# Kernel optimization log

Hardware: AMD Instinct MI355X
Metric: run time of the kernel (lower is better)

Reference implementation:

```python
import jax, jax.numpy as jnp
import numpy as np

B, N, NP, K, C_IN, C, H = 16, 4096, 1024, 32, 128, 256, 4
C_G = C_IN + 3  # grouped feature dim (use_xyz concat of relative coords)
EPS = 1e-3      # keras LayerNormalization default epsilon


def setup_inputs() -> dict:
    key = jax.random.key(0)
    ks = jax.random.split(key, 16)
    s = 0.05
    return {
        "xyz": jax.random.normal(ks[0], (B, N, 3), jnp.float32),
        "newxyz": jax.random.normal(ks[1], (B, NP, 3), jnp.float32),
        "feature_input": jax.random.normal(ks[2], (B, N, C_IN), jnp.float32),
        "w_qkv": jax.random.normal(ks[3], (C_G, 3 * C), jnp.float32) * s,
        "proj_w": jax.random.normal(ks[4], (C, C), jnp.float32) * s,
        "proj_b": jnp.zeros((C,), jnp.float32),
        "dense_w": jax.random.normal(ks[5], (C_G, C), jnp.float32) * s,
        "dense_b": jnp.zeros((C,), jnp.float32),
        "fc1_w": jax.random.normal(ks[6], (C, 2 * C), jnp.float32) * s,
        "fc1_b": jnp.zeros((2 * C,), jnp.float32),
        "fc2_w": jax.random.normal(ks[7], (2 * C, C), jnp.float32) * s,
        "fc2_b": jnp.zeros((C,), jnp.float32),
        "n1_g": jnp.ones((C_G,), jnp.float32),
        "n1_b": jnp.zeros((C_G,), jnp.float32),
        "n2_g": jnp.ones((C,), jnp.float32),
        "n2_b": jnp.zeros((C,), jnp.float32),
        "group_num": K,
        "training": True,
    }


def _layernorm(x, g, b):
    m = jnp.mean(x, axis=-1, keepdims=True)
    v = jnp.mean(jnp.square(x - m), axis=-1, keepdims=True)
    return (x - m) * jax.lax.rsqrt(v + EPS) * g + b


def _sample_and_group(newxyz, group_num, xyz, feats):
    # squared pairwise distances (B, NP, N)
    d2 = (jnp.sum(newxyz**2, -1)[:, :, None]
          - 2.0 * jnp.einsum('bpc,bnc->bpn', newxyz, xyz)
          + jnp.sum(xyz**2, -1)[:, None, :])
    _, idx = jax.lax.top_k(-d2, group_num)            # (B, NP, K) nearest
    b_idx = jnp.arange(newxyz.shape[0])[:, None, None]
    grouped_xyz = xyz[b_idx, idx] - newxyz[:, :, None, :]   # (B, NP, K, 3)
    grouped_feat = feats[b_idx, idx]                        # (B, NP, K, C_IN)
    return jnp.concatenate([grouped_xyz, grouped_feat], axis=-1)


def _self_attention(x, w_qkv, proj_w, proj_b):
    b, n, k = x.shape[0], x.shape[1], x.shape[2]
    d = C // H
    qkv = jnp.einsum('bnkc,cd->bnkd', x, w_qkv)
    qkv = qkv.reshape(b, n, k, 3, H, d)
    qkv = jnp.transpose(qkv, (3, 0, 1, 4, 2, 5))      # (3, B, NP, H, K, d)
    q, kk, v = qkv[0], qkv[1], qkv[2]
    qm = jnp.max(q, axis=-2, keepdims=True)           # (B, NP, H, 1, d)
    attn = jnp.einsum('bnhqd,bnhkd->bnhqk', qm, kk) * (C ** -0.5)
    attn = jax.nn.softmax(attn, axis=-1)
    out = jnp.einsum('bnhqk,bnhkd->bnhqd', attn, v)[..., 0, :]  # (B, NP, H, d)
    out = out.reshape(b, n, C)
    return jax.nn.relu(out @ proj_w + proj_b)


def reference(xyz, newxyz, feature_input, w_qkv, proj_w, proj_b, dense_w,
              dense_b, fc1_w, fc1_b, fc2_w, fc2_b, n1_g, n1_b, n2_g, n2_b,
              group_num, training):
    gf = _sample_and_group(newxyz, group_num, xyz, feature_input)  # (B,NP,K,C_G)
    feat = _self_attention(_layernorm(gf, n1_g, n1_b), w_qkv, proj_w, proj_b)
    feat = feat + jax.nn.relu(jnp.max(gf, axis=-2) @ dense_w + dense_b)
    f2 = _layernorm(feat, n2_g, n2_b)
    f2 = jax.nn.relu(f2 @ fc1_w + fc1_b)
    f2 = f2 @ fc2_w + fc2_b
    return f2 + feat
```

## Files before the change

### kernel.cpp

```cpp
#include <hip/hip_runtime.h>
#include <hip/hip_bf16.h>

typedef __hip_bfloat16 bf16;

#define Bn   16
#define Nn   4096
#define NPn  1024
#define Kn   32
#define CINn 128
#define CGn  131
#define Cn   256
#define Hn   4
#define KPAD 160
#define XBS  168
#define XFS2 136
#define GFS  136

typedef __attribute__((ext_vector_type(8))) short frag_ab;
typedef __attribute__((ext_vector_type(4))) float frag_cd;

__device__ __forceinline__ float b2f(bf16 x) { return __bfloat162float(x); }
__device__ __forceinline__ bf16  f2b(float x) { return __float2bfloat16(x); }
__device__ __forceinline__ short f2bs(float x) {
  union { bf16 h; short s; } u; u.h = __float2bfloat16(x); return u.s;
}
__device__ __forceinline__ float bs2f(short s) {
  union { short v; bf16 h; } u; u.v = s; return __bfloat162float(u.h);
}
__device__ __forceinline__ unsigned f2ord(float f) {
  unsigned u = __float_as_uint(f);
  return u ^ ((u >> 31) ? 0xffffffffu : 0x80000000u);
}

__global__ __launch_bounds__(256) void xyzw_prep_kernel(
    const float* __restrict__ xyz, float4* __restrict__ xyzw) {
  const int i = blockIdx.x * 256 + threadIdx.x;
  const float x = xyz[i*3 + 0];
  const float y = xyz[i*3 + 1];
  const float z = xyz[i*3 + 2];
  const float sx = __fadd_rn(__fadd_rn(__fmul_rn(x,x), __fmul_rn(y,y)),
                             __fmul_rn(z,z));
  xyzw[i] = make_float4(x, y, z, sx);
}

__global__ __launch_bounds__(256) void knn_kernel(const float4* __restrict__ xyzw,
                                                  const float* __restrict__ newxyz,
                                                  int* __restrict__ idx_out) {
  constexpr int CAP = 2048;
  __shared__ unsigned long long tmin[256];
  __shared__ __align__(16) unsigned long long cand[CAP + 4];
  __shared__ unsigned long long wtau[4];
  __shared__ unsigned long long wred[4];
  __shared__ int scnt;
  const int bp  = blockIdx.x;
  const int b   = bp >> 10;
  const int tid = threadIdx.x;
  const float qx = newxyz[bp*3 + 0];
  const float qy = newxyz[bp*3 + 1];
  const float qz = newxyz[bp*3 + 2];
  const float sn = __fadd_rn(__fadd_rn(__fmul_rn(qx,qx), __fmul_rn(qy,qy)),
                             __fmul_rn(qz,qz));
  const float4* xb = xyzw + (size_t)b * Nn;
  unsigned long long key[16];
  unsigned long long lmin = ~0ull;
  #pragma unroll
  for (int s = 0; s < 16; ++s) {
    const int n = s*256 + tid;
    const float4 xw = xb[n];
    const float dot = __fadd_rn(__fadd_rn(__fmul_rn(qx,xw.x), __fmul_rn(qy,xw.y)),
                                __fmul_rn(qz,xw.z));
    const float d2 = __fadd_rn(__fsub_rn(sn, __fmul_rn(2.0f, dot)), xw.w);
    key[s] = ((unsigned long long)f2ord(d2) << 32) | (unsigned)n;
    if (key[s] < lmin) lmin = key[s];
  }
  const int lane = tid & 63, wv = tid >> 6;

  if (tid == 0) scnt = 0;
  tmin[tid] = lmin;
  __syncthreads();

  {
    const unsigned long long* wt = &tmin[wv * 64];
    int rk = 0;
    #pragma unroll 8
    for (int j = 0; j < 64; ++j) rk += (wt[j] < lmin) ? 1 : 0;
    if (rk == 15) wtau[wv] = lmin;
  }
  __syncthreads();
  unsigned long long tau = wtau[0];
  if (wtau[1] < tau) tau = wtau[1];
  if (wtau[2] < tau) tau = wtau[2];
  if (wtau[3] < tau) tau = wtau[3];

  #pragma unroll
  for (int s = 0; s < 16; ++s) {
    if (key[s] <= tau) {
      const int p = atomicAdd(&scnt, 1);
      if (p < CAP) cand[p] = key[s];
    }
  }
  __syncthreads();
  const int m = scnt;

  if (m >= Kn && m <= CAP) {
    if (tid < 4) cand[m + tid] = ~0ull;
    __syncthreads();
    const int m4 = (m + 3) & ~3;
    for (int t = tid; t < m; t += 256) {
      const unsigned long long mykey = cand[t];
      int r = 0;
      for (int j = 0; j < m4; j += 4) {
        r += (cand[j+0] < mykey) ? 1 : 0;
        r += (cand[j+1] < mykey) ? 1 : 0;
        r += (cand[j+2] < mykey) ? 1 : 0;
        r += (cand[j+3] < mykey) ? 1 : 0;
      }
      if (r < Kn) idx_out[(size_t)bp*Kn + r] = (int)(mykey & 0xffffffffu);
    }
  } else {
    for (int s = 0; s < Kn; ++s) {
      unsigned long long mm = lmin;
      #pragma unroll
      for (int d = 32; d; d >>= 1) {
        const unsigned lo = __shfl_xor((unsigned)(mm & 0xffffffffu), d, 64);
        const unsigned hi = __shfl_xor((unsigned)(mm >> 32), d, 64);
        const unsigned long long o = ((unsigned long long)hi << 32) | lo;
        if (o < mm) mm = o;
      }
      if (lane == 0) wred[wv] = mm;
      __syncthreads();
      unsigned long long best = wred[0];
      if (wred[1] < best) best = wred[1];
      if (wred[2] < best) best = wred[2];
      if (wred[3] < best) best = wred[3];
      __syncthreads();
      const int n = (int)(best & 0xffffffffu);
      if (tid == 0) idx_out[(size_t)bp*Kn + s] = n;
      if ((n & 255) == tid) {
        const int slot = n >> 8;
        #pragma unroll
        for (int t = 0; t < 16; ++t) if (t == slot) key[t] = ~0ull;
        unsigned long long m2 = ~0ull;
        #pragma unroll
        for (int t = 0; t < 16; ++t) if (key[t] < m2) m2 = key[t];
        lmin = m2;
      }
    }
  }
}

__global__ __launch_bounds__(256) void wprep_all_kernel(
    const float* __restrict__ w_qkv, const float* __restrict__ proj_w,
    const float* __restrict__ dense_w, const float* __restrict__ fc1_w,
    const float* __restrict__ fc2_w, short* __restrict__ o_qkv,
    short* __restrict__ o_proj, short* __restrict__ o_dense,
    short* __restrict__ o_fc1, short* __restrict__ o_fc2) {
  const int blk = blockIdx.x;
  const float* W; short* out; int K, N, nnt, remap, base;
  if      (blk <  480) { W=w_qkv;   out=o_qkv;   K=CGn; N=768; nnt=48; remap=1; base=0;    }
  else if (blk <  736) { W=proj_w;  out=o_proj;  K=Cn;  N=256; nnt=16; remap=0; base=480;  }
  else if (blk <  896) { W=dense_w; out=o_dense; K=CGn; N=256; nnt=16; remap=1; base=736;  }
  else if (blk < 1408) { W=fc1_w;   out=o_fc1;   K=Cn;  N=512; nnt=32; remap=0; base=896;  }
  else                 { W=fc2_w;   out=o_fc2;   K=512; N=256; nnt=16; remap=0; base=1408; }
  const int t = (blk - base) * 256 + threadIdx.x;
  const int j    = t & 7;
  const int lane = (t >> 3) & 63;
  const int nt   = (t >> 9) % nnt;
  const int kt   = (t >> 9) / nnt;
  const int k = kt*32 + (lane >> 4)*8 + j;
  const int n = nt*16 + (lane & 15);
  int krow = k;
  if (remap) krow = (k < 128) ? k + 3 : k - 128;
  out[t] = (k < K) ? f2bs(W[(size_t)krow*N + n]) : (short)0;
}

__global__ __launch_bounds__(256, 3) void fused_attn_kernel(
    const float* __restrict__ xyz, const float* __restrict__ newxyz,
    const float* __restrict__ featin, const short* __restrict__ wfrag,
    const float* __restrict__ n1g, const float* __restrict__ n1b,
    const int* __restrict__ idx, bf16* __restrict__ attnout,
    bf16* __restrict__ gfmax) {
  __shared__ __align__(16) short Raw[64 * XFS2];
  __shared__ __align__(16) short Xs[64 * XBS];
  __shared__ float sg[CGn], sb[CGn];
  __shared__ int sidx[64];
  const int bp0 = blockIdx.x * 2;
  const int b   = bp0 >> 10;
  const int tid = threadIdx.x;
  if (tid < 64) {
    int n = idx[(size_t)bp0*Kn + tid];
    sidx[tid] = ((unsigned)n < (unsigned)Nn) ? n : 0;
  }
  if (tid < CGn) {
    const int rj = (tid < 128) ? tid + 3 : tid - 128;
    sg[tid] = n1g[rj];
    sb[tid] = n1b[rj];
  }
  __syncthreads();
  const int kk = tid >> 3, sub = tid & 7;
  const int lane = tid & 63, w = tid >> 6;
  const int col = lane & 15, quad = lane >> 4;
  float mean[2], rstd[2];
  {
    float4 r[2][4];
    float ex[2] = {0.f, 0.f};
    #pragma unroll
    for (int p = 0; p < 2; ++p) {
      const int row = p*32 + kk;
      const float* frow = featin + ((size_t)b*Nn + sidx[row])*CINn;
      #pragma unroll
      for (int i = 0; i < 4; ++i) r[p][i] = *(const float4*)(frow + sub*4 + 32*i);
      if (sub < 3)
        ex[p] = xyz[((size_t)b*Nn + sidx[row])*3 + sub] - newxyz[(bp0+p)*3 + sub];
    }
    #pragma unroll
    for (int p = 0; p < 2; ++p) {
      const int row = p*32 + kk;
      #pragma unroll
      for (int i = 0; i < 4; ++i) {
        short4 s4 = { f2bs(r[p][i].x), f2bs(r[p][i].y), f2bs(r[p][i].z), f2bs(r[p][i].w) };
        *(short4*)&Raw[row*XFS2 + sub*4 + 32*i] = s4;
      }
      if (sub < 3) Raw[row*XFS2 + 128 + sub] = f2bs(ex[p]);
    }
    #pragma unroll
    for (int p = 0; p < 2; ++p) {
      float s = ex[p], s2 = ex[p]*ex[p];
      #pragma unroll
      for (int i = 0; i < 4; ++i) {
        s  += r[p][i].x + r[p][i].y + r[p][i].z + r[p][i].w;
        s2 += r[p][i].x*r[p][i].x + r[p][i].y*r[p][i].y
            + r[p][i].z*r[p][i].z + r[p][i].w*r[p][i].w;
      }
      s  += __shfl_xor(s, 1, 64);  s  += __shfl_xor(s, 2, 64);  s  += __shfl_xor(s, 4, 64);
      s2 += __shfl_xor(s2, 1, 64); s2 += __shfl_xor(s2, 2, 64); s2 += __shfl_xor(s2, 4, 64);
      mean[p] = s * (1.0f/CGn);
      const float var = s2 * (1.0f/CGn) - mean[p]*mean[p];
      rstd[p] = rsqrtf(var + 1e-3f);
    }
  }
  __syncthreads();
  #pragma unroll
  for (int p = 0; p < 2; ++p) {
    if (tid < GFS) {
      float m = 0.f;
      if (tid < CGn) {
        m = -1e30f;
        #pragma unroll
        for (int k2 = 0; k2 < Kn; ++k2)
          m = fmaxf(m, bs2f(Raw[(p*32 + k2)*XFS2 + tid]));
      }
      gfmax[(size_t)(bp0+p)*GFS + tid] = f2b(m);
    }
  }
  #pragma unroll
  for (int p = 0; p < 2; ++p) {
    const int row = p*32 + kk;
    #pragma unroll
    for (int i = 0; i < 4; ++i) {
      const float4 g4 = *(const float4*)&sg[sub*4 + 32*i];
      const float4 b4 = *(const float4*)&sb[sub*4 + 32*i];
      const short4 rv = *(const short4*)&Raw[row*XFS2 + sub*4 + 32*i];
      short4 s4;
      s4.x = f2bs((bs2f(rv.x) - mean[p])*rstd[p]*g4.x + b4.x);
      s4.y = f2bs((bs2f(rv.y) - mean[p])*rstd[p]*g4.y + b4.y);
      s4.z = f2bs((bs2f(rv.z) - mean[p])*rstd[p]*g4.z + b4.z);
      s4.w = f2bs((bs2f(rv.w) - mean[p])*rstd[p]*g4.w + b4.w);
      *(short4*)&Xs[row*XBS + sub*4 + 32*i] = s4;
    }
    if (sub < 3) {
      const float rxv = bs2f(Raw[row*XFS2 + 128 + sub]);
      Xs[row*XBS + 128 + sub] = f2bs((rxv - mean[p])*rstd[p]*sg[128+sub] + sb[128+sub]);
    }
  }
  #pragma unroll
  for (int u = 0; u < 8; ++u) {
    const int e = u*256 + tid;
    const int row = e >> 5, jj = 131 + (e & 31);
    if (jj < 160) Xs[row*XBS + jj] = 0;
  }
  __syncthreads();
  float qm[2][4], aw[2][2][4], inv[2];
  {
    #pragma unroll 1
    for (int half = 0; half < 2; ++half) {
      frag_cd acc[2][4] = {};
      for (int kt = 0; kt < 5; ++kt) {
        const int ko = kt*32 + quad*8;
        frag_ab a[4];
        #pragma unroll
        for (int mt = 0; mt < 4; ++mt)
          a[mt] = *(const frag_ab*)&Xs[(mt*16 + col)*XBS + ko];
        #pragma unroll
        for (int ntl = 0; ntl < 2; ++ntl) {
          const int nt = w*4 + half*2 + ntl;
          const frag_ab bfr = *(const frag_ab*)(wfrag + ((size_t)(kt*48 + nt)*64 + lane)*8);
          #pragma unroll
          for (int mt = 0; mt < 4; ++mt)
            acc[ntl][mt] = __builtin_amdgcn_mfma_f32_16x16x32_bf16(a[mt], bfr, acc[ntl][mt], 0, 0, 0);
        }
      }
      #pragma unroll
      for (int p = 0; p < 2; ++p)
        #pragma unroll
        for (int ntl = 0; ntl < 2; ++ntl) {
          float m = -1e30f;
          #pragma unroll
          for (int mtl = 0; mtl < 2; ++mtl)
            #pragma unroll
            for (int rr = 0; rr < 4; ++rr) m = fmaxf(m, acc[ntl][p*2+mtl][rr]);
          m = fmaxf(m, __shfl_xor(m, 16, 64));
          m = fmaxf(m, __shfl_xor(m, 32, 64));
          qm[p][half*2 + ntl] = m;
        }
    }
  }
  {
    float pp[2][2][4] = {};
    #pragma unroll 1
    for (int half = 0; half < 2; ++half) {
      frag_cd acc[2][4] = {};
      for (int kt = 0; kt < 5; ++kt) {
        const int ko = kt*32 + quad*8;
        frag_ab a[4];
        #pragma unroll
        for (int mt = 0; mt < 4; ++mt)
          a[mt] = *(const frag_ab*)&Xs[(mt*16 + col)*XBS + ko];
        #pragma unroll
        for (int ntl = 0; ntl < 2; ++ntl) {
          const int nt = 16 + w*4 + half*2 + ntl;
          const frag_ab bfr = *(const frag_ab*)(wfrag + ((size_t)(kt*48 + nt)*64 + lane)*8);
          #pragma unroll
          for (int mt = 0; mt < 4; ++mt)
            acc[ntl][mt] = __builtin_amdgcn_mfma_f32_16x16x32_bf16(a[mt], bfr, acc[ntl][mt], 0, 0, 0);
        }
      }
      #pragma unroll
      for (int p = 0; p < 2; ++p)
        #pragma unroll
        for (int mtl = 0; mtl < 2; ++mtl)
          #pragma unroll
          for (int rr = 0; rr < 4; ++rr) {
            #pragma unroll
            for (int ntl = 0; ntl < 2; ++ntl)
              pp[p][mtl][rr] = fmaf(qm[p][half*2 + ntl], acc[ntl][p*2+mtl][rr], pp[p][mtl][rr]);
          }
    }
    #pragma unroll
    for (int p = 0; p < 2; ++p) {
      float lg[2][4];
      #pragma unroll
      for (int mtl = 0; mtl < 2; ++mtl)
        #pragma unroll
        for (int rr = 0; rr < 4; ++rr) {
          float v = pp[p][mtl][rr];
          #pragma unroll
          for (int d = 1; d < 16; d <<= 1) v += __shfl_xor(v, d, 64);
          lg[mtl][rr] = v * 0.0625f;
        }
      float mx = -1e30f;
      #pragma unroll
      for (int mtl = 0; mtl < 2; ++mtl)
        #pragma unroll
        for (int rr = 0; rr < 4; ++rr) mx = fmaxf(mx, lg[mtl][rr]);
      mx = fmaxf(mx, __shfl_xor(mx, 16, 64));
      mx = fmaxf(mx, __shfl_xor(mx, 32, 64));
      float ssum = 0.f;
      #pragma unroll
      for (int mtl = 0; mtl < 2; ++mtl)
        #pragma unroll
        for (int rr = 0; rr < 4; ++rr) { aw[p][mtl][rr] = expf(lg[mtl][rr] - mx); ssum += aw[p][mtl][rr]; }
      ssum += __shfl_xor(ssum, 16, 64);
      ssum += __shfl_xor(ssum, 32, 64);
      inv[p] = 1.f / ssum;
    }
  }
  {
    #pragma unroll 1
    for (int half = 0; half < 2; ++half) {
      frag_cd acc[2][4] = {};
      for (int kt = 0; kt < 5; ++kt) {
        const int ko = kt*32 + quad*8;
        frag_ab a[4];
        #pragma unroll
        for (int mt = 0; mt < 4; ++mt)
          a[mt] = *(const frag_ab*)&Xs[(mt*16 + col)*XBS + ko];
        #pragma unroll
        for (int ntl = 0; ntl < 2; ++ntl) {
          const int nt = 32 + w*4 + half*2 + ntl;
          const frag_ab bfr = *(const frag_ab*)(wfrag + ((size_t)(kt*48 + nt)*64 + lane)*8);
          #pragma unroll
          for (int mt = 0; mt < 4; ++mt)
            acc[ntl][mt] = __builtin_amdgcn_mfma_f32_16x16x32_bf16(a[mt], bfr, acc[ntl][mt], 0, 0, 0);
        }
      }
      #pragma unroll
      for (int p = 0; p < 2; ++p)
        #pragma unroll
        for (int ntl = 0; ntl < 2; ++ntl) {
          float o = 0.f;
          #pragma unroll
          for (int mtl = 0; mtl < 2; ++mtl)
            #pragma unroll
            for (int rr = 0; rr < 4; ++rr) o = fmaf(aw[p][mtl][rr], acc[ntl][p*2+mtl][rr], o);
          o += __shfl_xor(o, 16, 64);
          o += __shfl_xor(o, 32, 64);
          if (quad == 0)
            attnout[(size_t)(bp0+p)*Cn + w*64 + (half*2 + ntl)*16 + col] = f2b(o * inv[p]);
        }
    }
  }
}

template<bool RELU, bool ADD_S, bool OUT_BF16>
__global__ __launch_bounds__(256) void mfma_gemm_kernel(
    const bf16* __restrict__ A, int lda, int Ka,
    const short* __restrict__ Wf, int nnt_total, int N,
    const float* __restrict__ bias, const bf16* __restrict__ S,
    void* __restrict__ Dv) {
  __shared__ __align__(16) short As[64*40];
  const int m0 = blockIdx.y * 64;
  const int n0 = blockIdx.x * 128;
  const int tid = threadIdx.x, lane = tid & 63, w = tid >> 6;
  const int col = lane & 15, quad = lane >> 4;
  const int row = tid >> 2, c8 = (tid & 3) * 8;
  frag_cd acc[4][2] = {};
  const int nkt = (Ka + 31) >> 5;
  for (int kt = 0; kt < nkt; ++kt) {
    const int k0 = kt*32 + c8;
    frag_ab av = {0,0,0,0,0,0,0,0};
    if (k0 + 8 <= Ka)
      av = *(const frag_ab*)((const short*)A + (size_t)(m0+row)*lda + k0);
    __syncthreads();
    *(frag_ab*)&As[row*40 + c8] = av;
    __syncthreads();
    frag_ab afr[4];
    #pragma unroll
    for (int mt = 0; mt < 4; ++mt)
      afr[mt] = *(const frag_ab*)&As[(mt*16 + col)*40 + quad*8];
    #pragma unroll
    for (int ntl = 0; ntl < 2; ++ntl) {
      const int nt = (n0 >> 4) + w*2 + ntl;
      const frag_ab bfr = *(const frag_ab*)(Wf + ((size_t)(kt*nnt_total + nt)*64 + lane)*8);
      #pragma unroll
      for (int mt = 0; mt < 4; ++mt)
        acc[mt][ntl] = __builtin_amdgcn_mfma_f32_16x16x32_bf16(afr[mt], bfr, acc[mt][ntl], 0, 0, 0);
    }
  }
  #pragma unroll
  for (int ntl = 0; ntl < 2; ++ntl) {
    const int n = n0 + w*32 + ntl*16 + col;
    const float bv = bias[n];
    #pragma unroll
    for (int mt = 0; mt < 4; ++mt) {
      #pragma unroll
      for (int r = 0; r < 4; ++r) {
        const int m = m0 + mt*16 + quad*4 + r;
        float v = acc[mt][ntl][r] + bv;
        if (RELU) v = fmaxf(v, 0.f);
        if (ADD_S) v += b2f(S[(size_t)m*N + n]);
        if (OUT_BF16) ((bf16*)Dv)[(size_t)m*N + n] = f2b(v);
        else          ((float*)Dv)[(size_t)m*N + n] = v;
      }
    }
  }
}

__global__ __launch_bounds__(256) void dual_gemm_kernel(
    const bf16* __restrict__ A1, const short* __restrict__ W1,
    const bf16* __restrict__ A2, const short* __restrict__ W2,
    const float* __restrict__ b1, const float* __restrict__ b2,
    bf16* __restrict__ D) {
  __shared__ __align__(16) short As[64*40];
  const int m0 = blockIdx.y * 64;
  const int n0 = blockIdx.x * 128;
  const int tid = threadIdx.x, lane = tid & 63, w = tid >> 6;
  const int col = lane & 15, quad = lane >> 4;
  const int row = tid >> 2, c8 = (tid & 3) * 8;
  frag_cd acc1[4][2] = {}, acc2[4][2] = {};
  for (int kt = 0; kt < 8; ++kt) {
    const frag_ab av = *(const frag_ab*)((const short*)A1 + (size_t)(m0+row)*Cn + kt*32 + c8);
    __syncthreads();
    *(frag_ab*)&As[row*40 + c8] = av;
    __syncthreads();
    frag_ab afr[4];
    #pragma unroll
    for (int mt = 0; mt < 4; ++mt)
      afr[mt] = *(const frag_ab*)&As[(mt*16 + col)*40 + quad*8];
    #pragma unroll
    for (int ntl = 0; ntl < 2; ++ntl) {
      const int nt = (n0 >> 4) + w*2 + ntl;
      const frag_ab bfr = *(const frag_ab*)(W1 + ((size_t)(kt*16 + nt)*64 + lane)*8);
      #pragma unroll
      for (int mt = 0; mt < 4; ++mt)
        acc1[mt][ntl] = __builtin_amdgcn_mfma_f32_16x16x32_bf16(afr[mt], bfr, acc1[mt][ntl], 0, 0, 0);
    }
  }
  for (int kt = 0; kt < 5; ++kt) {
    const int k0 = kt*32 + c8;
    frag_ab av = {0,0,0,0,0,0,0,0};
    if (k0 + 8 <= GFS)
      av = *(const frag_ab*)((const short*)A2 + (size_t)(m0+row)*GFS + k0);
    __syncthreads();
    *(frag_ab*)&As[row*40 + c8] = av;
    __syncthreads();
    frag_ab afr[4];
    #pragma unroll
    for (int mt = 0; mt < 4; ++mt)
      afr[mt] = *(const frag_ab*)&As[(mt*16 + col)*40 + quad*8];
    #pragma unroll
    for (int ntl = 0; ntl < 2; ++ntl) {
      const int nt = (n0 >> 4) + w*2 + ntl;
      const frag_ab bfr = *(const frag_ab*)(W2 + ((size_t)(kt*16 + nt)*64 + lane)*8);
      #pragma unroll
      for (int mt = 0; mt < 4; ++mt)
        acc2[mt][ntl] = __builtin_amdgcn_mfma_f32_16x16x32_bf16(afr[mt], bfr, acc2[mt][ntl], 0, 0, 0);
    }
  }
  #pragma unroll
  for (int ntl = 0; ntl < 2; ++ntl) {
    const int n = n0 + w*32 + ntl*16 + col;
    const float bv1 = b1[n], bv2 = b2[n];
    #pragma unroll
    for (int mt = 0; mt < 4; ++mt) {
      #pragma unroll
      for (int r = 0; r < 4; ++r) {
        const int m = m0 + mt*16 + quad*4 + r;
        const float v = fmaxf(acc1[mt][ntl][r] + bv1, 0.f)
                      + fmaxf(acc2[mt][ntl][r] + bv2, 0.f);
        D[(size_t)m*Cn + n] = f2b(v);
      }
    }
  }
}

__global__ __launch_bounds__(256) void ln2_kernel(const bf16* __restrict__ feat,
                                                  const float* __restrict__ g,
                                                  const float* __restrict__ b,
                                                  bf16* __restrict__ out) {
  const int r = blockIdx.x*4 + (threadIdx.x >> 6), lane = threadIdx.x & 63;
  float vv[4];
  #pragma unroll
  for (int c = 0; c < 4; ++c) vv[c] = b2f(feat[(size_t)r*Cn + lane*4 + c]);
  float s  = vv[0] + vv[1] + vv[2] + vv[3];
  float s2 = vv[0]*vv[0] + vv[1]*vv[1] + vv[2]*vv[2] + vv[3]*vv[3];
  #pragma unroll
  for (int d = 32; d; d >>= 1) { s += __shfl_xor(s, d, 64); s2 += __shfl_xor(s2, d, 64); }
  const float mean = s * (1.f/256.f);
  const float var  = s2 * (1.f/256.f) - mean*mean;
  const float rstd = rsqrtf(var + 1e-3f);
  #pragma unroll
  for (int c = 0; c < 4; ++c) {
    const int cc = lane*4 + c;
    out[(size_t)r*Cn + cc] = f2b((vv[c] - mean)*rstd*g[cc] + b[cc]);
  }
}

extern "C" void kernel_launch(void* const* d_in, const int* in_sizes, int n_in,
                              void* d_out, int out_size, void* d_ws, size_t ws_size,
                              hipStream_t stream) {
  const float* xyz     = (const float*)d_in[0];
  const float* newxyz  = (const float*)d_in[1];
  const float* featin  = (const float*)d_in[2];
  const float* w_qkv   = (const float*)d_in[3];
  const float* proj_w  = (const float*)d_in[4];
  const float* proj_b  = (const float*)d_in[5];
  const float* dense_w = (const float*)d_in[6];
  const float* dense_b = (const float*)d_in[7];
  const float* fc1_w   = (const float*)d_in[8];
  const float* fc1_b   = (const float*)d_in[9];
  const float* fc2_w   = (const float*)d_in[10];
  const float* fc2_b   = (const float*)d_in[11];
  const float* n1g     = (const float*)d_in[12];
  const float* n1b     = (const float*)d_in[13];
  const float* n2g     = (const float*)d_in[14];
  const float* n2b     = (const float*)d_in[15];

  char*  ws     = (char*)d_ws;
  short* wqkv   = (short*)(ws + 0);
  short* wproj  = (short*)(ws + 245760);
  short* wdense = (short*)(ws + 376832);
  short* wfc1   = (short*)(ws + 458752);
  short* wfc2   = (short*)(ws + 720896);
  bf16*  featB  = (bf16*)(ws + 1048576);
  bf16*  attnA  = (bf16*)(ws + 9437184);
  bf16*  gfmax  = (bf16*)(ws + 17825792);
  int*   idxws  = (int*) (ws + 22282240);
  bf16*  fc1out = (bf16*)(ws + 24379392);
  float4* xyzw  = (float4*)(ws + 24379392);

  const int M = Bn * NPn;

  xyzw_prep_kernel<<<dim3(Bn*Nn/256), dim3(256), 0, stream>>>(xyz, xyzw);
  knn_kernel<<<dim3(M), dim3(256), 0, stream>>>(xyzw, newxyz, idxws);
  wprep_all_kernel<<<dim3(1920), dim3(256), 0, stream>>>(
      w_qkv, proj_w, dense_w, fc1_w, fc2_w, wqkv, wproj, wdense, wfc1, wfc2);

  fused_attn_kernel<<<dim3(M/2), dim3(256), 0, stream>>>(
      xyz, newxyz, featin, wqkv, n1g, n1b, idxws, attnA, gfmax);
  dual_gemm_kernel<<<dim3(2, M/64), dim3(256), 0, stream>>>(
      attnA, wproj, gfmax, wdense, proj_b, dense_b, featB);
  ln2_kernel<<<dim3(M/4), dim3(256), 0, stream>>>(featB, n2g, n2b, attnA);
  mfma_gemm_kernel<true, false, true><<<dim3(4, M/64), dim3(256), 0, stream>>>(
      attnA, Cn, Cn, wfc1, 32, 512, fc1_b, (const bf16*)nullptr, fc1out);
  mfma_gemm_kernel<false, true, false><<<dim3(2, M/64), dim3(256), 0, stream>>>(
      fc1out, 512, 512, wfc2, 16, Cn, fc2_b, featB, d_out);
}
```

Baseline: 421.2 us.

## Batch eight queries per KNN block and drop separate raw LDS buffer

The KNN kernel now handles eight query points per block and keeps the batch's 4096 reference points in registers across those queries, so the point data is loaded once per block rather than once per query. In the fused attention kernel, the separate Raw LDS buffer is removed: raw bf16 features are staged in Xs for the group-max, and the layernorm is then computed from the fp32 values held in registers, with an extra barrier before Xs is overwritten. This lowers LDS usage and may raise occupancy, and the layernorm input is now fp32 instead of bf16-rounded. The costs are more register pressure (16 float4 per thread in KNN), fewer KNN blocks to spread across the GPU, and queries inside a block running one after another.

```diff
diff --git a/kernel.cpp b/kernel.cpp
--- a/kernel.cpp
+++ b/kernel.cpp
@@ -15,6 +15,7 @@
 #define XBS  168
 #define XFS2 136
 #define GFS  136
+#define KNNG 8
 
 typedef __attribute__((ext_vector_type(8))) short frag_ab;
 typedef __attribute__((ext_vector_type(4))) float frag_cd;
@@ -52,99 +53,108 @@
   __shared__ unsigned long long wtau[4];
   __shared__ unsigned long long wred[4];
   __shared__ int scnt;
-  const int bp  = blockIdx.x;
-  const int b   = bp >> 10;
+  const int bp0 = blockIdx.x * KNNG;
+  const int b   = bp0 >> 10;
   const int tid = threadIdx.x;
-  const float qx = newxyz[bp*3 + 0];
-  const float qy = newxyz[bp*3 + 1];
-  const float qz = newxyz[bp*3 + 2];
-  const float sn = __fadd_rn(__fadd_rn(__fmul_rn(qx,qx), __fmul_rn(qy,qy)),
-                             __fmul_rn(qz,qz));
+  const int lane = tid & 63, wv = tid >> 6;
   const float4* xb = xyzw + (size_t)b * Nn;
-  unsigned long long key[16];
-  unsigned long long lmin = ~0ull;
-  #pragma unroll
-  for (int s = 0; s < 16; ++s) {
-    const int n = s*256 + tid;
-    const float4 xw = xb[n];
-    const float dot = __fadd_rn(__fadd_rn(__fmul_rn(qx,xw.x), __fmul_rn(qy,xw.y)),
-                                __fmul_rn(qz,xw.z));
-    const float d2 = __fadd_rn(__fsub_rn(sn, __fmul_rn(2.0f, dot)), xw.w);
-    key[s] = ((unsigned long long)f2ord(d2) << 32) | (unsigned)n;
-    if (key[s] < lmin) lmin = key[s];
-  }
-  const int lane = tid & 63, wv = tid >> 6;
-
-  if (tid == 0) scnt = 0;
-  tmin[tid] = lmin;
-  __syncthreads();
-
-  {
-    const unsigned long long* wt = &tmin[wv * 64];
-    int rk = 0;
-    #pragma unroll 8
-    for (int j = 0; j < 64; ++j) rk += (wt[j] < lmin) ? 1 : 0;
-    if (rk == 15) wtau[wv] = lmin;
-  }
-  __syncthreads();
-  unsigned long long tau = wtau[0];
-  if (wtau[1] < tau) tau = wtau[1];
-  if (wtau[2] < tau) tau = wtau[2];
-  if (wtau[3] < tau) tau = wtau[3];
-
-  #pragma unroll
-  for (int s = 0; s < 16; ++s) {
-    if (key[s] <= tau) {
-      const int p = atomicAdd(&scnt, 1);
-      if (p < CAP) cand[p] = key[s];
-    }
-  }
-  __syncthreads();
-  const int m = scnt;
-
-  if (m >= Kn && m <= CAP) {
-    if (tid < 4) cand[m + tid] = ~0ull;
-    __syncthreads();
-    const int m4 = (m + 3) & ~3;
-    for (int t = tid; t < m; t += 256) {
-      const unsigned long long mykey = cand[t];
-      int r = 0;
-      for (int j = 0; j < m4; j += 4) {
-        r += (cand[j+0] < mykey) ? 1 : 0;
-        r += (cand[j+1] < mykey) ? 1 : 0;
-        r += (cand[j+2] < mykey) ? 1 : 0;
-        r += (cand[j+3] < mykey) ? 1 : 0;
-      }
-      if (r < Kn) idx_out[(size_t)bp*Kn + r] = (int)(mykey & 0xffffffffu);
-    }
-  } else {
-    for (int s = 0; s < Kn; ++s) {
-      unsigned long long mm = lmin;
-      #pragma unroll
-      for (int d = 32; d; d >>= 1) {
-        const unsigned lo = __shfl_xor((unsigned)(mm & 0xffffffffu), d, 64);
-        const unsigned hi = __shfl_xor((unsigned)(mm >> 32), d, 64);
-        const unsigned long long o = ((unsigned long long)hi << 32) | lo;
-        if (o < mm) mm = o;
-      }
-      if (lane == 0) wred[wv] = mm;
+
+  float4 pt[16];
+  #pragma unroll
+  for (int s = 0; s < 16; ++s) pt[s] = xb[s*256 + tid];
+
+  #pragma unroll 1
+  for (int g = 0; g < KNNG; ++g) {
+    const int bp = bp0 + g;
+    const float qx = newxyz[bp*3 + 0];
+    const float qy = newxyz[bp*3 + 1];
+    const float qz = newxyz[bp*3 + 2];
+    const float sn = __fadd_rn(__fadd_rn(__fmul_rn(qx,qx), __fmul_rn(qy,qy)),
+                               __fmul_rn(qz,qz));
+    unsigned long long key[16];
+    unsigned long long lmin = ~0ull;
+    #pragma unroll
+    for (int s = 0; s < 16; ++s) {
+      const int n = s*256 + tid;
+      const float dot = __fadd_rn(__fadd_rn(__fmul_rn(qx,pt[s].x), __fmul_rn(qy,pt[s].y)),
+                                  __fmul_rn(qz,pt[s].z));
+      const float d2 = __fadd_rn(__fsub_rn(sn, __fmul_rn(2.0f, dot)), pt[s].w);
+      key[s] = ((unsigned long long)f2ord(d2) << 32) | (unsigned)n;
+      if (key[s] < lmin) lmin = key[s];
+    }
+
+    if (tid == 0) scnt = 0;
+    tmin[tid] = lmin;
+    __syncthreads();
+
+    {
+      const unsigned long long* wt = &tmin[wv * 64];
+      int rk = 0;
+      #pragma unroll 8
+      for (int j = 0; j < 64; ++j) rk += (wt[j] < lmin) ? 1 : 0;
+      if (rk == 15) wtau[wv] = lmin;
+    }
+    __syncthreads();
+    unsigned long long tau = wtau[0];
+    if (wtau[1] < tau) tau = wtau[1];
+    if (wtau[2] < tau) tau = wtau[2];
+    if (wtau[3] < tau) tau = wtau[3];
+
+    #pragma unroll
+    for (int s = 0; s < 16; ++s) {
+      if (key[s] <= tau) {
+        const int p = atomicAdd(&scnt, 1);
+        if (p < CAP) cand[p] = key[s];
+      }
+    }
+    __syncthreads();
+    const int m = scnt;
+
+    if (m >= Kn && m <= CAP) {
+      if (tid < 4) cand[m + tid] = ~0ull;
       __syncthreads();
-      unsigned long long best = wred[0];
-      if (wred[1] < best) best = wred[1];
-      if (wred[2] < best) best = wred[2];
-      if (wred[3] < best) best = wred[3];
+      const int m4 = (m + 3) & ~3;
+      for (int t = tid; t < m; t += 256) {
+        const unsigned long long mykey = cand[t];
+        int r = 0;
+        for (int j = 0; j < m4; j += 4) {
+          r += (cand[j+0] < mykey) ? 1 : 0;
+          r += (cand[j+1] < mykey) ? 1 : 0;
+          r += (cand[j+2] < mykey) ? 1 : 0;
+          r += (cand[j+3] < mykey) ? 1 : 0;
+        }
+        if (r < Kn) idx_out[(size_t)bp*Kn + r] = (int)(mykey & 0xffffffffu);
+      }
+    } else {
+      for (int s = 0; s < Kn; ++s) {
+        unsigned long long mm = lmin;
+        #pragma unroll
+        for (int d = 32; d; d >>= 1) {
+          const unsigned lo = __shfl_xor((unsigned)(mm & 0xffffffffu), d, 64);
+          const unsigned hi = __shfl_xor((unsigned)(mm >> 32), d, 64);
+          const unsigned long long o = ((unsigned long long)hi << 32) | lo;
+          if (o < mm) mm = o;
+        }
+        if (lane == 0) wred[wv] = mm;
+        __syncthreads();
+        unsigned long long best = wred[0];
+        if (wred[1] < best) best = wred[1];
+        if (wred[2] < best) best = wred[2];
+        if (wred[3] < best) best = wred[3];
+        __syncthreads();
+        const int n = (int)(best & 0xffffffffu);
+        if (tid == 0) idx_out[(size_t)bp*Kn + s] = n;
+        if ((n & 255) == tid) {
+          const int slot = n >> 8;
+          #pragma unroll
+          for (int t = 0; t < 16; ++t) if (t == slot) key[t] = ~0ull;
+          unsigned long long m2 = ~0ull;
+          #pragma unroll
+          for (int t = 0; t < 16; ++t) if (key[t] < m2) m2 = key[t];
+          lmin = m2;
+        }
+      }
       __syncthreads();
-      const int n = (int)(best & 0xffffffffu);
-      if (tid == 0) idx_out[(size_t)bp*Kn + s] = n;
-      if ((n & 255) == tid) {
-        const int slot = n >> 8;
-        #pragma unroll
-        for (int t = 0; t < 16; ++t) if (t == slot) key[t] = ~0ull;
-        unsigned long long m2 = ~0ull;
-        #pragma unroll
-        for (int t = 0; t < 16; ++t) if (key[t] < m2) m2 = key[t];
-        lmin = m2;
-      }
     }
   }
 }
@@ -180,7 +190,6 @@
     const float* __restrict__ n1g, const float* __restrict__ n1b,
     const int* __restrict__ idx, bf16* __restrict__ attnout,
     bf16* __restrict__ gfmax) {
-  __shared__ __align__(16) short Raw[64 * XFS2];
   __shared__ __align__(16) short Xs[64 * XBS];
   __shared__ float sg[CGn], sb[CGn];
   __shared__ int sidx[64];
@@ -198,46 +207,42 @@
   }
   __syncthreads();
   const int kk = tid >> 3, sub = tid & 7;
-  const int lane = tid & 63, w = tid >> 6;
-  const int col = lane & 15, quad = lane >> 4;
+  float4 r[2][4];
+  float ex[2] = {0.f, 0.f};
+  #pragma unroll
+  for (int p = 0; p < 2; ++p) {
+    const int row = p*32 + kk;
+    const float* frow = featin + ((size_t)b*Nn + sidx[row])*CINn;
+    #pragma unroll
+    for (int i = 0; i < 4; ++i) r[p][i] = *(const float4*)(frow + sub*4 + 32*i);
+    if (sub < 3)
+      ex[p] = xyz[((size_t)b*Nn + sidx[row])*3 + sub] - newxyz[(bp0+p)*3 + sub];
+  }
+  #pragma unroll
+  for (int p = 0; p < 2; ++p) {
+    const int row = p*32 + kk;
+    #pragma unroll
+    for (int i = 0; i < 4; ++i) {
+      short4 s4 = { f2bs(r[p][i].x), f2bs(r[p][i].y), f2bs(r[p][i].z), f2bs(r[p][i].w) };
+      *(short4*)&Xs[row*XFS2 + sub*4 + 32*i] = s4;
+    }
+    if (sub < 3) Xs[row*XFS2 + 128 + sub] = f2bs(ex[p]);
+  }
   float mean[2], rstd[2];
-  {
-    float4 r[2][4];
-    float ex[2] = {0.f, 0.f};
-    #pragma unroll
-    for (int p = 0; p < 2; ++p) {
-      const int row = p*32 + kk;
-      const float* frow = featin + ((size_t)b*Nn + sidx[row])*CINn;
-      #pragma unroll
-      for (int i = 0; i < 4; ++i) r[p][i] = *(const float4*)(frow + sub*4 + 32*i);
-      if (sub < 3)
-        ex[p] = xyz[((size_t)b*Nn + sidx[row])*3 + sub] - newxyz[(bp0+p)*3 + sub];
-    }
-    #pragma unroll
-    for (int p = 0; p < 2; ++p) {
-      const int row = p*32 + kk;
-      #pragma unroll
-      for (int i = 0; i < 4; ++i) {
-        short4 s4 = { f2bs(r[p][i].x), f2bs(r[p][i].y), f2bs(r[p][i].z), f2bs(r[p][i].w) };
-        *(short4*)&Raw[row*XFS2 + sub*4 + 32*i] = s4;
-      }
-      if (sub < 3) Raw[row*XFS2 + 128 + sub] = f2bs(ex[p]);
-    }
-    #pragma unroll
-    for (int p = 0; p < 2; ++p) {
-      float s = ex[p], s2 = ex[p]*ex[p];
-      #pragma unroll
-      for (int i = 0; i < 4; ++i) {
-        s  += r[p][i].x + r[p][i].y + r[p][i].z + r[p][i].w;
-        s2 += r[p][i].x*r[p][i].x + r[p][i].y*r[p][i].y
-            + r[p][i].z*r[p][i].z + r[p][i].w*r[p][i].w;
-      }
-      s  += __shfl_xor(s, 1, 64);  s  += __shfl_xor(s, 2, 64);  s  += __shfl_xor(s, 4, 64);
-      s2 += __shfl_xor(s2, 1, 64); s2 += __shfl_xor(s2, 2, 64); s2 += __shfl_xor(s2, 4, 64);
-      mean[p] = s * (1.0f/CGn);
-      const float var = s2 * (1.0f/CGn) - mean[p]*mean[p];
-      rstd[p] = rsqrtf(var + 1e-3f);
-    }
+  #pragma unroll
+  for (int p = 0; p < 2; ++p) {
+    float s = ex[p], s2 = ex[p]*ex[p];
+    #pragma unroll
+    for (int i = 0; i < 4; ++i) {
+      s  += r[p][i].x + r[p][i].y + r[p][i].z + r[p][i].w;
+      s2 += r[p][i].x*r[p][i].x + r[p][i].y*r[p][i].y
+          + r[p][i].z*r[p][i].z + r[p][i].w*r[p][i].w;
+    }
+    s  += __shfl_xor(s, 1, 64);  s  += __shfl_xor(s, 2, 64);  s  += __shfl_xor(s, 4, 64);
+    s2 += __shfl_xor(s2, 1, 64); s2 += __shfl_xor(s2, 2, 64); s2 += __shfl_xor(s2, 4, 64);
+    mean[p] = s * (1.0f/CGn);
+    const float var = s2 * (1.0f/CGn) - mean[p]*mean[p];
+    rstd[p] = rsqrtf(var + 1e-3f);
   }
   __syncthreads();
   #pragma unroll
@@ -248,11 +253,12 @@
         m = -1e30f;
         #pragma unroll
         for (int k2 = 0; k2 < Kn; ++k2)
-          m = fmaxf(m, bs2f(Raw[(p*32 + k2)*XFS2 + tid]));
+          m = fmaxf(m, bs2f(Xs[(p*32 + k2)*XFS2 + tid]));
       }
       gfmax[(size_t)(bp0+p)*GFS + tid] = f2b(m);
     }
   }
+  __syncthreads();
   #pragma unroll
   for (int p = 0; p < 2; ++p) {
     const int row = p*32 + kk;
@@ -260,18 +266,15 @@
     for (int i = 0; i < 4; ++i) {
       const float4 g4 = *(const float4*)&sg[sub*4 + 32*i];
       const float4 b4 = *(const float4*)&sb[sub*4 + 32*i];
-      const short4 rv = *(const short4*)&Raw[row*XFS2 + sub*4 + 32*i];
       short4 s4;
-      s4.x = f2bs((bs2f(rv.x) - mean[p])*rstd[p]*g4.x + b4.x);
-      s4.y = f2bs((bs2f(rv.y) - mean[p])*rstd[p]*g4.y + b4.y);
-      s4.z = f2bs((bs2f(rv.z) - mean[p])*rstd[p]*g4.z + b4.z);
-      s4.w = f2bs((bs2f(rv.w) - mean[p])*rstd[p]*g4.w + b4.w);
+      s4.x = f2bs((r[p][i].x - mean[p])*rstd[p]*g4.x + b4.x);
+      s4.y = f2bs((r[p][i].y - mean[p])*rstd[p]*g4.y + b4.y);
+      s4.z = f2bs((r[p][i].z - mean[p])*rstd[p]*g4.z + b4.z);
+      s4.w = f2bs((r[p][i].w - mean[p])*rstd[p]*g4.w + b4.w);
       *(short4*)&Xs[row*XBS + sub*4 + 32*i] = s4;
     }
-    if (sub < 3) {
-      const float rxv = bs2f(Raw[row*XFS2 + 128 + sub]);
-      Xs[row*XBS + 128 + sub] = f2bs((rxv - mean[p])*rstd[p]*sg[128+sub] + sb[128+sub]);
-    }
+    if (sub < 3)
+      Xs[row*XBS + 128 + sub] = f2bs((ex[p] - mean[p])*rstd[p]*sg[128+sub] + sb[128+sub]);
   }
   #pragma unroll
   for (int u = 0; u < 8; ++u) {
@@ -280,6 +283,8 @@
     if (jj < 160) Xs[row*XBS + jj] = 0;
   }
   __syncthreads();
+  const int lane = tid & 63, w = tid >> 6;
+  const int col = lane & 15, quad = lane >> 4;
   float qm[2][4], aw[2][2][4], inv[2];
   {
     #pragma unroll 1
@@ -592,7 +597,7 @@
   const int M = Bn * NPn;
 
   xyzw_prep_kernel<<<dim3(Bn*Nn/256), dim3(256), 0, stream>>>(xyz, xyzw);
-  knn_kernel<<<dim3(M), dim3(256), 0, stream>>>(xyzw, newxyz, idxws);
+  knn_kernel<<<dim3(M/KNNG), dim3(256), 0, stream>>>(xyzw, newxyz, idxws);
   wprep_all_kernel<<<dim3(1920), dim3(256), 0, stream>>>(
       w_qkv, proj_w, dense_w, fc1_w, fc2_w, wqkv, wproj, wdense, wfc1, wfc2);
 
```

Result: slower. 450.8 us (+7.0%).
